# Kernel optimization log

Measured on AMD Instinct MI355X. Metric: run time of the kernel, lower is better.

The kernel has to match this reference:

```python
import jax, jax.numpy as jnp
import numpy as np

DIM = 1024
NUM_HEADS = 16
HEAD_DIM = DIM // NUM_HEADS
EPS_NORM = 1e-12  # F.normalize eps
EPS_LN = 1e-5     # nn.LayerNorm eps


def setup_inputs() -> dict:
    key = jax.random.key(0)
    ks = jax.random.split(key, 6)
    x = jax.random.normal(ks[0], (4, 2048, DIM), dtype=jnp.float32)
    # LayerNorm params
    ln_w = jnp.ones((DIM,), jnp.float32)
    ln_b = jnp.zeros((DIM,), jnp.float32)
    # qkv: xavier_uniform on weight [3D, D], zero bias
    limit = float(np.sqrt(6.0 / (DIM + 3 * DIM)))
    qkv_w = jax.random.uniform(ks[1], (3 * DIM, DIM), jnp.float32, -limit, limit)
    qkv_b = jnp.zeros((3 * DIM,), jnp.float32)
    # out_proj: normal std=0.02, zero bias
    out_w = 0.02 * jax.random.normal(ks[2], (DIM, DIM), dtype=jnp.float32)
    out_b = jnp.zeros((DIM,), jnp.float32)
    return {"x": x, "ln_w": ln_w, "ln_b": ln_b, "qkv_w": qkv_w,
            "qkv_b": qkv_b, "out_w": out_w, "out_b": out_b}


def reference(x, ln_w, ln_b, qkv_w, qkv_b, out_w, out_b):
    B, N, D = x.shape
    # pre-LayerNorm
    mu = jnp.mean(x, axis=-1, keepdims=True)
    var = jnp.mean(jnp.square(x - mu), axis=-1, keepdims=True)
    h = (x - mu) / jnp.sqrt(var + EPS_LN) * ln_w + ln_b
    # QKV projection (torch Linear: y = h @ W^T + b)
    qkv = h @ qkv_w.T + qkv_b                     # [B, N, 3D]
    qkv = qkv.reshape(B, N, 3, NUM_HEADS, HEAD_DIM)
    q, k, v = (jnp.transpose(qkv[:, :, i], (0, 2, 1, 3)) for i in range(3))  # [B,H,N,hd]
    # per-head L2 normalize (F.normalize semantics: x / max(||x||, eps))
    q = q / jnp.maximum(jnp.linalg.norm(q, axis=-1, keepdims=True), EPS_NORM)
    k = k / jnp.maximum(jnp.linalg.norm(k, axis=-1, keepdims=True), EPS_NORM)
    scale = HEAD_DIM ** 0.5
    attn = jnp.einsum('bhqd,bhkd->bhqk', q, k) * scale
    attn = jax.nn.softmax(attn, axis=-1)
    out = jnp.einsum('bhqk,bhkd->bhqd', attn, v)  # [B,H,N,hd]
    out = jnp.transpose(out, (0, 2, 1, 3)).reshape(B, N, D)
    return x + out @ out_w.T + out_b
```

## Files before the change

kernel.cpp:

```cpp
#include <hip/hip_runtime.h>
#include <math.h>

constexpr int D     = 1024;
constexpr int NH    = 16;
constexpr int HD    = 64;
constexpr int SEQ   = 2048;
constexpr int BATCH = 4;
constexpr int NTOK  = BATCH * SEQ;

typedef short s16x8 __attribute__((ext_vector_type(8)));
typedef short s16x4 __attribute__((ext_vector_type(4)));
typedef float f32x4 __attribute__((ext_vector_type(4)));
typedef unsigned short u16;
typedef unsigned int   u32;

#if __has_builtin(__builtin_amdgcn_exp2f)
#define EXP2(x) __builtin_amdgcn_exp2f(x)
#else
#define EXP2(x) exp2f(x)
#endif

__device__ __forceinline__ short f2bf(float f) {
    unsigned u = __float_as_uint(f);
    unsigned r = (u + 0x7FFFu + ((u >> 16) & 1u)) >> 16;
    return (short)r;
}
__device__ __forceinline__ float bf2f(u16 s) {
    return __uint_as_float(((unsigned)s) << 16);
}

__device__ __forceinline__ u32 pack_bf16_pair(float f0, float f1) {
    u32 a = __float_as_uint(f1) + 0x8000u;
    u32 b = __float_as_uint(f0) + 0x8000u;
    return __builtin_amdgcn_perm(a, b, 0x07060302u);
}

__device__ __forceinline__ void async_lds16(const void* g, void* l) {
    __builtin_amdgcn_global_load_lds(
        (const __attribute__((address_space(1))) unsigned int*)g,
        (__attribute__((address_space(3))) unsigned int*)l, 16, 0, 0);
}

__device__ __forceinline__ float block_reduce_sum(float v, float* red) {
    int lane = threadIdx.x & 63, wid = threadIdx.x >> 6;
    #pragma unroll
    for (int off = 32; off > 0; off >>= 1) v += __shfl_down(v, off, 64);
    if (lane == 0) red[wid] = v;
    __syncthreads();
    float r = red[0] + red[1] + red[2] + red[3];
    __syncthreads();
    return r;
}

__global__ __launch_bounds__(256) void ln_kernel(const float* __restrict__ x,
                                                 const float* __restrict__ w,
                                                 const float* __restrict__ b,
                                                 u16* __restrict__ h) {
    __shared__ float red[4];
    int row = blockIdx.x;
    const float* xr = x + (size_t)row * D;
    int t = threadIdx.x;
    float v[4];
    float s = 0.f;
    #pragma unroll
    for (int i = 0; i < 4; i++) { v[i] = xr[t + 256 * i]; s += v[i]; }
    float mean = block_reduce_sum(s, red) * (1.0f / 1024.0f);
    float ss = 0.f;
    #pragma unroll
    for (int i = 0; i < 4; i++) { float d = v[i] - mean; ss += d * d; }
    float var = block_reduce_sum(ss, red) * (1.0f / 1024.0f);
    float rstd = rsqrtf(var + 1e-5f);
    u16* hr = h + (size_t)row * D;
    #pragma unroll
    for (int i = 0; i < 4; i++) {
        int c = t + 256 * i;
        hr[c] = (u16)f2bf((v[i] - mean) * rstd * w[c] + b[c]);
    }
}

__global__ __launch_bounds__(256) void cast_kernel(const float* __restrict__ in,
                                                   u16* __restrict__ out, int n) {
    int i = (blockIdx.x * 256 + threadIdx.x) * 4;
    if (i >= n) return;
    float4 f = *(const float4*)(in + i);
    s16x4 o4;
    o4[0] = f2bf(f.x); o4[1] = f2bf(f.y); o4[2] = f2bf(f.z); o4[3] = f2bf(f.w);
    *(s16x4*)(out + i) = o4;
}

template <typename OutT, bool RES, bool NORMK>
__global__ __launch_bounds__(256) void gemm_bf16(const u16* __restrict__ A,
                                                 const u16* __restrict__ B,
                                                 const float* __restrict__ bias,
                                                 const float* __restrict__ R,
                                                 OutT* __restrict__ C,
                                                 int M, int N, int K) {
    __shared__ u16 As[128 * 32];
    __shared__ u16 Bs[128 * 32];
    int tid = threadIdx.x, wave = tid >> 6, lane = tid & 63;
    int quad = lane >> 4, l16 = lane & 15;
    int wm = (wave & 1) * 64, wn = (wave >> 1) * 64;
    int rowBase = blockIdx.y * 128, colBase = blockIdx.x * 128;

    int srow = lane >> 2;
    int sk8  = (lane & 3) * 8;

    f32x4 acc[4][4];
    #pragma unroll
    for (int i = 0; i < 4; i++)
        #pragma unroll
        for (int j = 0; j < 4; j++)
            acc[i][j] = (f32x4){0.f, 0.f, 0.f, 0.f};

    for (int k0 = 0; k0 < K; k0 += 32) {
        __syncthreads();
        #pragma unroll
        for (int i = 0; i < 2; i++) {
            int r = wave * 32 + i * 16;
            const u16* ga = A + (size_t)(rowBase + r + srow) * K + k0 + sk8;
            async_lds16(ga, &As[r * 32]);
            const u16* gb = B + (size_t)(colBase + r + srow) * K + k0 + sk8;
            async_lds16(gb, &Bs[r * 32]);
        }
        __syncthreads();

        s16x8 af[4], bfr[4];
        #pragma unroll
        for (int t = 0; t < 4; t++) {
            af[t]  = *(const s16x8*)&As[(wm + t * 16 + l16) * 32 + quad * 8];
            bfr[t] = *(const s16x8*)&Bs[(wn + t * 16 + l16) * 32 + quad * 8];
        }
        #pragma unroll
        for (int mt = 0; mt < 4; mt++)
            #pragma unroll
            for (int nt = 0; nt < 4; nt++)
                acc[mt][nt] = __builtin_amdgcn_mfma_f32_16x16x32_bf16(
                    af[mt], bfr[nt], acc[mt][nt], 0, 0, 0);
    }

    bool normk = NORMK && (colBase + wn) >= 1024 && (colBase + wn) < 2048;

    #pragma unroll
    for (int mt = 0; mt < 4; mt++) {
        float vals[4][4];
        #pragma unroll
        for (int nt = 0; nt < 4; nt++) {
            int gn = colBase + wn + nt * 16 + l16;
            float bv = bias[gn];
            #pragma unroll
            for (int r = 0; r < 4; r++) {
                float val = acc[mt][nt][r] + bv;
                if (RES) {
                    int gm = rowBase + wm + mt * 16 + quad * 4 + r;
                    val += R[(size_t)gm * N + gn];
                }
                vals[nt][r] = val;
            }
        }
        if (normk) {
            #pragma unroll
            for (int r = 0; r < 4; r++) {
                float ssq = 0.f;
                #pragma unroll
                for (int nt = 0; nt < 4; nt++) ssq = fmaf(vals[nt][r], vals[nt][r], ssq);
                ssq += __shfl_xor(ssq, 1, 64);
                ssq += __shfl_xor(ssq, 2, 64);
                ssq += __shfl_xor(ssq, 4, 64);
                ssq += __shfl_xor(ssq, 8, 64);
                float inv = 1.0f / fmaxf(sqrtf(ssq), 1e-12f);
                #pragma unroll
                for (int nt = 0; nt < 4; nt++) vals[nt][r] *= inv;
            }
        }
        #pragma unroll
        for (int nt = 0; nt < 4; nt++) {
            int gn = colBase + wn + nt * 16 + l16;
            int gm0 = rowBase + wm + mt * 16 + quad * 4;
            #pragma unroll
            for (int r = 0; r < 4; r++) {
                if constexpr (sizeof(OutT) == 2)
                    C[(size_t)(gm0 + r) * N + gn] = (OutT)f2bf(vals[nt][r]);
                else
                    C[(size_t)(gm0 + r) * N + gn] = vals[nt][r];
            }
        }
    }
}

__global__ __launch_bounds__(256, 2) void mha_kernel(const u16* __restrict__ qkv,
                                                     u16* __restrict__ out) {
    __shared__ u16 Ks[64 * 64];
    constexpr int VS = 68;
    __shared__ u16 Vt[64 * VS];

    int bh = blockIdx.x & 63;
    int qt = blockIdx.x >> 6;
    int b  = bh >> 4, h = bh & 15;
    int tid = threadIdx.x;
    int wave = tid >> 6, lane = tid & 63;
    int quad = lane >> 4, l16 = lane & 15;

    const size_t rs = 3072;
    constexpr float SCL = 11.5415605f;

    s16x8 aq[4][2];
    #pragma unroll
    for (int rt = 0; rt < 4; rt++) {
        const u16* qb = qkv + ((size_t)(b * SEQ) + qt * 256 + wave * 64 + rt * 16 + l16) * rs + h * 64;
        s16x8 r0 = *(const s16x8*)(qb + quad * 8);
        s16x8 r1 = *(const s16x8*)(qb + 32 + quad * 8);
        float f0[8], f1[8], ss = 0.f;
        #pragma unroll
        for (int i = 0; i < 8; i++) { f0[i] = bf2f((u16)r0[i]); ss = fmaf(f0[i], f0[i], ss); }
        #pragma unroll
        for (int i = 0; i < 8; i++) { f1[i] = bf2f((u16)r1[i]); ss = fmaf(f1[i], f1[i], ss); }
        ss += __shfl_xor(ss, 16, 64);
        ss += __shfl_xor(ss, 32, 64);
        float inv = SCL / fmaxf(sqrtf(ss), 1e-12f);
        #pragma unroll
        for (int i = 0; i < 8; i++) {
            aq[rt][0][i] = f2bf(f0[i] * inv);
            aq[rt][1][i] = f2bf(f1[i] * inv);
        }
    }

    const f32x4 cinit = {-SCL, -SCL, -SCL, -SCL};
    f32x4 o2[4][4];
    f32x4 osum[4];
    #pragma unroll
    for (int rt = 0; rt < 4; rt++) {
        #pragma unroll
        for (int ht = 0; ht < 4; ht++) o2[rt][ht] = (f32x4){0.f, 0.f, 0.f, 0.f};
        osum[rt] = (f32x4){0.f, 0.f, 0.f, 0.f};
    }
    s16x8 ones;
    #pragma unroll
    for (int i = 0; i < 8; i++) ones[i] = (short)0x3F80;

    int skey = tid >> 2, c4 = tid & 3;
    int ksw  = skey & 7;
    int vp2 = tid >> 3, dc = (tid & 7) * 8;
    const u16* kglob  = qkv + ((size_t)(b * SEQ) + skey) * rs + 1024 + h * 64 + c4 * 16;
    const u16* vglob0 = qkv + ((size_t)(b * SEQ) + 2 * vp2) * rs + 2048 + h * 64 + dc;
    u16* kdst0 = &Ks[skey * 64 + ((2 * c4)     ^ ksw) * 8];
    u16* kdst1 = &Ks[skey * 64 + ((2 * c4 + 1) ^ ksw) * 8];
    u32* vt32 = (u32*)&Vt[0];

    s16x8 kr0 = ((const s16x8*)kglob)[0];
    s16x8 kr1 = ((const s16x8*)kglob)[1];
    s16x8 vr0 = *(const s16x8*)(vglob0);
    s16x8 vr1 = *(const s16x8*)(vglob0 + rs);

    int swz = l16 & 7;

    for (int kb = 0; kb < SEQ / 64; kb++) {
        __syncthreads();
        *(s16x8*)kdst0 = kr0;
        *(s16x8*)kdst1 = kr1;
        #pragma unroll
        for (int i = 0; i < 8; i++) {
            u32 pk = (u32)(u16)vr0[i] | ((u32)(u16)vr1[i] << 16);
            vt32[(dc + i) * (VS / 2) + vp2] = pk;
        }
        __syncthreads();

        if (kb < SEQ / 64 - 1) {
            const u16* kp = kglob + (size_t)(kb + 1) * 64 * rs;
            const u16* vp = vglob0 + (size_t)(kb + 1) * 64 * rs;
            kr0 = ((const s16x8*)kp)[0];
            kr1 = ((const s16x8*)kp)[1];
            vr0 = *(const s16x8*)(vp);
            vr1 = *(const s16x8*)(vp + rs);
        }

        s16x4 pfr[4][4];
        #pragma unroll
        for (int t = 0; t < 4; t++) {
            const u16* krow = &Ks[(t * 16 + l16) * 64];
            s16x8 bk0 = *(const s16x8*)(krow + ((0 + quad) ^ swz) * 8);
            s16x8 bk1 = *(const s16x8*)(krow + ((4 + quad) ^ swz) * 8);
            #pragma unroll
            for (int rt = 0; rt < 4; rt++) {
                f32x4 s = cinit;
                s = __builtin_amdgcn_mfma_f32_16x16x32_bf16(bk0, aq[rt][0], s, 0, 0, 0);
                s = __builtin_amdgcn_mfma_f32_16x16x32_bf16(bk1, aq[rt][1], s, 0, 0, 0);
                uint2 pk2;
                pk2.x = pack_bf16_pair(EXP2(s[0]), EXP2(s[1]));
                pk2.y = pack_bf16_pair(EXP2(s[2]), EXP2(s[3]));
                pfr[rt][t] = __builtin_bit_cast(s16x4, pk2);
            }
        }

        #pragma unroll
        for (int pr = 0; pr < 2; pr++) {
            int tA = pr * 2, tB = pr * 2 + 1;
            s16x8 bp[4];
            #pragma unroll
            for (int rt = 0; rt < 4; rt++)
                bp[rt] = __builtin_shufflevector(pfr[rt][tA], pfr[rt][tB],
                                                 0, 1, 2, 3, 4, 5, 6, 7);
            #pragma unroll
            for (int ht = 0; ht < 4; ht++) {
                const u16* vrow = &Vt[(ht * 16 + l16) * VS];
                s16x4 va = *(const s16x4*)(vrow + tA * 16 + quad * 4);
                s16x4 vb = *(const s16x4*)(vrow + tB * 16 + quad * 4);
                s16x8 vfr = __builtin_shufflevector(va, vb, 0, 1, 2, 3, 4, 5, 6, 7);
                #pragma unroll
                for (int rt = 0; rt < 4; rt++)
                    o2[rt][ht] = __builtin_amdgcn_mfma_f32_16x16x32_bf16(
                        vfr, bp[rt], o2[rt][ht], 0, 0, 0);
            }
            #pragma unroll
            for (int rt = 0; rt < 4; rt++)
                osum[rt] = __builtin_amdgcn_mfma_f32_16x16x32_bf16(
                    ones, bp[rt], osum[rt], 0, 0, 0);
        }
    }

    #pragma unroll
    for (int rt = 0; rt < 4; rt++) {
        float inv = 1.0f / osum[rt][0];
        int orow = b * SEQ + qt * 256 + wave * 64 + rt * 16 + l16;
        u16* op = out + (size_t)orow * D + h * 64 + quad * 4;
        #pragma unroll
        for (int ht = 0; ht < 4; ht++) {
            f32x4 v = o2[rt][ht];
            u32 lo = pack_bf16_pair(v[0] * inv, v[1] * inv);
            u32 hi = pack_bf16_pair(v[2] * inv, v[3] * inv);
            uint2 pk = {lo, hi};
            *(uint2*)(op + ht * 16) = pk;
        }
    }
}

extern "C" void kernel_launch(void* const* d_in, const int* in_sizes, int n_in,
                              void* d_out, int out_size, void* d_ws, size_t ws_size,
                              hipStream_t stream) {
    const float* x     = (const float*)d_in[0];
    const float* ln_w  = (const float*)d_in[1];
    const float* ln_b  = (const float*)d_in[2];
    const float* qkv_w = (const float*)d_in[3];
    const float* qkv_b = (const float*)d_in[4];
    const float* out_w = (const float*)d_in[5];
    const float* out_b = (const float*)d_in[6];
    float* y = (float*)d_out;

    char* ws = (char*)d_ws;
    u16* qkv = (u16*)ws;
    u16* h   = (u16*)(ws + (size_t)48 * 1024 * 1024);
    u16* wq  = (u16*)(ws + (size_t)64 * 1024 * 1024);
    u16* wo  = (u16*)(ws + (size_t)70 * 1024 * 1024);
    u16* attn_out = h;

    ln_kernel<<<NTOK, 256, 0, stream>>>(x, ln_w, ln_b, h);
    cast_kernel<<<(3 * D * D) / 1024, 256, 0, stream>>>(qkv_w, wq, 3 * D * D);
    cast_kernel<<<(D * D) / 1024, 256, 0, stream>>>(out_w, wo, D * D);

    {
        dim3 grid(3 * D / 128, NTOK / 128);
        gemm_bf16<u16, false, true><<<grid, 256, 0, stream>>>(h, wq, qkv_b, nullptr,
                                                              qkv, NTOK, 3 * D, D);
    }

    mha_kernel<<<BATCH * NH * (SEQ / 256), 256, 0, stream>>>(qkv, attn_out);

    {
        dim3 grid(D / 128, NTOK / 128);
        gemm_bf16<float, true, false><<<grid, 256, 0, stream>>>(attn_out, wo, out_b,
                                                                x, y, NTOK, D, D);
    }
}
```

Measured before the change: 294.8 us.

## Replace 128x128 GEMM with 256x256 double-buffered pipelined GEMM with swizzled LDS

Replaces the simple 128x128-tile bf16 GEMM, which synchronizes on every K step, with a 512-thread 256x256-tile kernel. It uses double-buffered LDS with async global-to-LDS prefetch two K tiles ahead, an XOR-swizzled LDS layout to avoid bank conflicts, raised wave priority around the MFMA phases, and a block-index swizzle for L2 locality. The goal is to hide load latency and improve data reuse in the QKV and output projections. In exchange the kernel has many more accumulator registers, uses a large LDS footprint (128KB), and launches far fewer blocks.

```diff
diff --git a/kernel.cpp b/kernel.cpp
--- a/kernel.cpp
+++ b/kernel.cpp
@@ -88,73 +88,182 @@
     *(s16x4*)(out + i) = o4;
 }
 
+__device__ __forceinline__ s16x8 rdfrag(const u16* lds, int row, int kk, int quad) {
+    int byte = row * 128 + ((kk * 64 + quad * 16) ^ ((row & 7) << 4));
+    return *(const s16x8*)((const char*)lds + byte);
+}
+
+__device__ __forceinline__ void stage_half_A(const u16* __restrict__ A, u16* ldsA,
+                                             int rowBase, int K, int kt, int hs,
+                                             int wave, int lane) {
+    #pragma unroll
+    for (int i = 0; i < 2; i++) {
+        int c = wave * 2 + i;
+        int baserow = ((c & 7) * 8) + ((c >> 3) << 7) + (hs << 6);
+        int row = baserow + (lane >> 3);
+        int colb = ((lane & 7) * 16) ^ ((row & 7) << 4);
+        const u16* src = A + (size_t)(rowBase + row) * K + kt * 64 + (colb >> 1);
+        async_lds16(src, ldsA + baserow * 64);
+    }
+}
+__device__ __forceinline__ void stage_half_B(const u16* __restrict__ B, u16* ldsB,
+                                             int colBase, int K, int kt, int hs,
+                                             int wave, int lane) {
+    #pragma unroll
+    for (int i = 0; i < 2; i++) {
+        int c = wave * 2 + i;
+        int baserow = ((c & 3) * 8) + ((c >> 2) << 6) + (hs << 5);
+        int row = baserow + (lane >> 3);
+        int colb = ((lane & 7) * 16) ^ ((row & 7) << 4);
+        const u16* src = B + (size_t)(colBase + row) * K + kt * 64 + (colb >> 1);
+        async_lds16(src, ldsB + baserow * 64);
+    }
+}
+
 template <typename OutT, bool RES, bool NORMK>
-__global__ __launch_bounds__(256) void gemm_bf16(const u16* __restrict__ A,
-                                                 const u16* __restrict__ B,
-                                                 const float* __restrict__ bias,
-                                                 const float* __restrict__ R,
-                                                 OutT* __restrict__ C,
-                                                 int M, int N, int K) {
-    __shared__ u16 As[128 * 32];
-    __shared__ u16 Bs[128 * 32];
+__global__ __launch_bounds__(512, 2) void gemm256(const u16* __restrict__ A,
+                                                  const u16* __restrict__ B,
+                                                  const float* __restrict__ bias,
+                                                  const float* __restrict__ R,
+                                                  OutT* __restrict__ C,
+                                                  int M, int N, int K) {
+    __shared__ u16 lds[2][2][256 * 64];
+
+    int nby = M >> 8;
+    int cpx = gridDim.x >> 3;
+    int bid = blockIdx.x;
+    int swz = (bid & 7) * cpx + (bid >> 3);
+    int bx = swz / nby, by = swz % nby;
+    int rowBase = by << 8, colBase = bx << 8;
+
     int tid = threadIdx.x, wave = tid >> 6, lane = tid & 63;
     int quad = lane >> 4, l16 = lane & 15;
-    int wm = (wave & 1) * 64, wn = (wave >> 1) * 64;
-    int rowBase = blockIdx.y * 128, colBase = blockIdx.x * 128;
-
-    int srow = lane >> 2;
-    int sk8  = (lane & 3) * 8;
-
-    f32x4 acc[4][4];
-    #pragma unroll
-    for (int i = 0; i < 4; i++)
-        #pragma unroll
-        for (int j = 0; j < 4; j++)
-            acc[i][j] = (f32x4){0.f, 0.f, 0.f, 0.f};
-
-    for (int k0 = 0; k0 < K; k0 += 32) {
-        __syncthreads();
-        #pragma unroll
-        for (int i = 0; i < 2; i++) {
-            int r = wave * 32 + i * 16;
-            const u16* ga = A + (size_t)(rowBase + r + srow) * K + k0 + sk8;
-            async_lds16(ga, &As[r * 32]);
-            const u16* gb = B + (size_t)(colBase + r + srow) * K + k0 + sk8;
-            async_lds16(gb, &Bs[r * 32]);
-        }
-        __syncthreads();
-
-        s16x8 af[4], bfr[4];
-        #pragma unroll
-        for (int t = 0; t < 4; t++) {
-            af[t]  = *(const s16x8*)&As[(wm + t * 16 + l16) * 32 + quad * 8];
-            bfr[t] = *(const s16x8*)&Bs[(wn + t * 16 + l16) * 32 + quad * 8];
-        }
-        #pragma unroll
-        for (int mt = 0; mt < 4; mt++)
-            #pragma unroll
-            for (int nt = 0; nt < 4; nt++)
-                acc[mt][nt] = __builtin_amdgcn_mfma_f32_16x16x32_bf16(
-                    af[mt], bfr[nt], acc[mt][nt], 0, 0, 0);
-    }
-
-    bool normk = NORMK && (colBase + wn) >= 1024 && (colBase + wn) < 2048;
-
-    #pragma unroll
-    for (int mt = 0; mt < 4; mt++) {
+    int wr = wave >> 2, wc = wave & 3;
+    int KT = K >> 6;
+
+    f32x4 acc[8][4];
+    #pragma unroll
+    for (int m = 0; m < 8; m++)
+        #pragma unroll
+        for (int n = 0; n < 4; n++)
+            acc[m][n] = (f32x4){0.f, 0.f, 0.f, 0.f};
+
+    stage_half_A(A, &lds[0][0][0], rowBase, K, 0, 0, wave, lane);
+    stage_half_B(B, &lds[0][1][0], colBase, K, 0, 0, wave, lane);
+    stage_half_A(A, &lds[0][0][0], rowBase, K, 0, 1, wave, lane);
+    stage_half_B(B, &lds[0][1][0], colBase, K, 0, 1, wave, lane);
+    stage_half_A(A, &lds[1][0][0], rowBase, K, 1, 0, wave, lane);
+    stage_half_B(B, &lds[1][1][0], colBase, K, 1, 0, wave, lane);
+    stage_half_A(A, &lds[1][0][0], rowBase, K, 1, 1, wave, lane);
+    asm volatile("s_waitcnt vmcnt(6)" ::: "memory");
+    __builtin_amdgcn_s_barrier();
+
+    for (int t = 0; t < KT; ++t) {
+        int bsel = t & 1;
+        u16* cA = &lds[bsel][0][0];
+        u16* cB = &lds[bsel][1][0];
+        u16* oB = &lds[bsel ^ 1][1][0];
+        int t1 = t + 1; if (t1 >= KT) t1 -= KT;
+        int t2 = t + 2; if (t2 >= KT) t2 -= KT;
+
+        s16x8 af[4][2], bf0[2][2], bf1[2][2];
+
+        #pragma unroll
+        for (int m = 0; m < 4; m++)
+            #pragma unroll
+            for (int kk = 0; kk < 2; kk++)
+                af[m][kk] = rdfrag(cA, wr * 128 + m * 16 + l16, kk, quad);
+        #pragma unroll
+        for (int n = 0; n < 2; n++)
+            #pragma unroll
+            for (int kk = 0; kk < 2; kk++)
+                bf0[n][kk] = rdfrag(cB, wc * 64 + n * 16 + l16, kk, quad);
+        stage_half_B(B, oB, colBase, K, t1, 1, wave, lane);
+        __builtin_amdgcn_s_barrier();
+        __builtin_amdgcn_s_setprio(1);
+        #pragma unroll
+        for (int kk = 0; kk < 2; kk++)
+            #pragma unroll
+            for (int m = 0; m < 4; m++)
+                #pragma unroll
+                for (int n = 0; n < 2; n++)
+                    acc[m][n] = __builtin_amdgcn_mfma_f32_16x16x32_bf16(
+                        af[m][kk], bf0[n][kk], acc[m][n], 0, 0, 0);
+        __builtin_amdgcn_s_setprio(0);
+        __builtin_amdgcn_s_barrier();
+
+        #pragma unroll
+        for (int n = 0; n < 2; n++)
+            #pragma unroll
+            for (int kk = 0; kk < 2; kk++)
+                bf1[n][kk] = rdfrag(cB, wc * 64 + (n + 2) * 16 + l16, kk, quad);
+        stage_half_A(A, cA, rowBase, K, t2, 0, wave, lane);
+        __builtin_amdgcn_s_barrier();
+        __builtin_amdgcn_s_setprio(1);
+        #pragma unroll
+        for (int kk = 0; kk < 2; kk++)
+            #pragma unroll
+            for (int m = 0; m < 4; m++)
+                #pragma unroll
+                for (int n = 0; n < 2; n++)
+                    acc[m][n + 2] = __builtin_amdgcn_mfma_f32_16x16x32_bf16(
+                        af[m][kk], bf1[n][kk], acc[m][n + 2], 0, 0, 0);
+        __builtin_amdgcn_s_setprio(0);
+        __builtin_amdgcn_s_barrier();
+
+        #pragma unroll
+        for (int m = 0; m < 4; m++)
+            #pragma unroll
+            for (int kk = 0; kk < 2; kk++)
+                af[m][kk] = rdfrag(cA, wr * 128 + (m + 4) * 16 + l16, kk, quad);
+        stage_half_B(B, cB, colBase, K, t2, 0, wave, lane);
+        __builtin_amdgcn_s_barrier();
+        __builtin_amdgcn_s_setprio(1);
+        #pragma unroll
+        for (int kk = 0; kk < 2; kk++)
+            #pragma unroll
+            for (int m = 0; m < 4; m++)
+                #pragma unroll
+                for (int n = 0; n < 2; n++)
+                    acc[m + 4][n] = __builtin_amdgcn_mfma_f32_16x16x32_bf16(
+                        af[m][kk], bf0[n][kk], acc[m + 4][n], 0, 0, 0);
+        __builtin_amdgcn_s_setprio(0);
+        __builtin_amdgcn_s_barrier();
+
+        stage_half_A(A, cA, rowBase, K, t2, 1, wave, lane);
+        __builtin_amdgcn_s_barrier();
+        __builtin_amdgcn_s_setprio(1);
+        #pragma unroll
+        for (int kk = 0; kk < 2; kk++)
+            #pragma unroll
+            for (int m = 0; m < 4; m++)
+                #pragma unroll
+                for (int n = 0; n < 2; n++)
+                    acc[m + 4][n + 2] = __builtin_amdgcn_mfma_f32_16x16x32_bf16(
+                        af[m][kk], bf1[n][kk], acc[m + 4][n + 2], 0, 0, 0);
+        __builtin_amdgcn_s_setprio(0);
+        asm volatile("s_waitcnt vmcnt(6)" ::: "memory");
+        __builtin_amdgcn_s_barrier();
+    }
+    asm volatile("s_waitcnt vmcnt(0)" ::: "memory");
+
+    bool normk = NORMK && (colBase + wc * 64) >= 1024 && (colBase + wc * 64) < 2048;
+
+    #pragma unroll
+    for (int m = 0; m < 8; m++) {
         float vals[4][4];
         #pragma unroll
-        for (int nt = 0; nt < 4; nt++) {
-            int gn = colBase + wn + nt * 16 + l16;
+        for (int n = 0; n < 4; n++) {
+            int gn = colBase + wc * 64 + n * 16 + l16;
             float bv = bias[gn];
             #pragma unroll
             for (int r = 0; r < 4; r++) {
-                float val = acc[mt][nt][r] + bv;
+                float val = acc[m][n][r] + bv;
                 if (RES) {
-                    int gm = rowBase + wm + mt * 16 + quad * 4 + r;
+                    int gm = rowBase + wr * 128 + m * 16 + quad * 4 + r;
                     val += R[(size_t)gm * N + gn];
                 }
-                vals[nt][r] = val;
+                vals[n][r] = val;
             }
         }
         if (normk) {
@@ -162,26 +271,26 @@
             for (int r = 0; r < 4; r++) {
                 float ssq = 0.f;
                 #pragma unroll
-                for (int nt = 0; nt < 4; nt++) ssq = fmaf(vals[nt][r], vals[nt][r], ssq);
+                for (int n = 0; n < 4; n++) ssq = fmaf(vals[n][r], vals[n][r], ssq);
                 ssq += __shfl_xor(ssq, 1, 64);
                 ssq += __shfl_xor(ssq, 2, 64);
                 ssq += __shfl_xor(ssq, 4, 64);
                 ssq += __shfl_xor(ssq, 8, 64);
                 float inv = 1.0f / fmaxf(sqrtf(ssq), 1e-12f);
                 #pragma unroll
-                for (int nt = 0; nt < 4; nt++) vals[nt][r] *= inv;
+                for (int n = 0; n < 4; n++) vals[n][r] *= inv;
             }
         }
         #pragma unroll
-        for (int nt = 0; nt < 4; nt++) {
-            int gn = colBase + wn + nt * 16 + l16;
-            int gm0 = rowBase + wm + mt * 16 + quad * 4;
+        for (int n = 0; n < 4; n++) {
+            int gn = colBase + wc * 64 + n * 16 + l16;
+            int gm0 = rowBase + wr * 128 + m * 16 + quad * 4;
             #pragma unroll
             for (int r = 0; r < 4; r++) {
                 if constexpr (sizeof(OutT) == 2)
-                    C[(size_t)(gm0 + r) * N + gn] = (OutT)f2bf(vals[nt][r]);
+                    C[(size_t)(gm0 + r) * N + gn] = (OutT)f2bf(vals[n][r]);
                 else
-                    C[(size_t)(gm0 + r) * N + gn] = vals[nt][r];
+                    C[(size_t)(gm0 + r) * N + gn] = vals[n][r];
             }
         }
     }
@@ -356,17 +465,11 @@
     cast_kernel<<<(3 * D * D) / 1024, 256, 0, stream>>>(qkv_w, wq, 3 * D * D);
     cast_kernel<<<(D * D) / 1024, 256, 0, stream>>>(out_w, wo, D * D);
 
-    {
-        dim3 grid(3 * D / 128, NTOK / 128);
-        gemm_bf16<u16, false, true><<<grid, 256, 0, stream>>>(h, wq, qkv_b, nullptr,
-                                                              qkv, NTOK, 3 * D, D);
-    }
+    gemm256<u16, false, true><<<(3 * D / 256) * (NTOK / 256), 512, 0, stream>>>(
+        h, wq, qkv_b, nullptr, qkv, NTOK, 3 * D, D);
 
     mha_kernel<<<BATCH * NH * (SEQ / 256), 256, 0, stream>>>(qkv, attn_out);
 
-    {
-        dim3 grid(D / 128, NTOK / 128);
-        gemm_bf16<float, true, false><<<grid, 256, 0, stream>>>(attn_out, wo, out_b,
-                                                                x, y, NTOK, D, D);
-    }
-}
+    gemm256<float, true, false><<<(D / 256) * (NTOK / 256), 512, 0, stream>>>(
+        attn_out, wo, out_b, x, y, NTOK, D, D);
+}
```

Measured after the change: 290.1 us. Within noise of the previous version (-1.6%).
